# Kernel optimization log

Measured on AMD Instinct MI355X. Metric: run time of the kernel, lower is better.

The kernel has to match this reference:

```python
import jax, jax.numpy as jnp
import numpy as np

COORD_DIM = 4
HIDDEN = 256
N_HIDDEN_LAYERS = 4  # num_layers - 1 hidden->hidden layers after the first
MIN_OMEGA = 10.0
MAX_OMEGA = 100.0
MEDIAN_OMEGA = (MIN_OMEGA + MAX_OMEGA) / 2.0
N = 524288


def _uniform(key, shape, bound):
    return jax.random.uniform(key, shape, jnp.float32, -bound, bound)


def setup_inputs() -> dict:
    key = jax.random.key(0)
    ks = jax.random.split(key, 16)
    coords = jax.random.normal(ks[0], (N, COORD_DIM), jnp.float32)
    # omega predictor: Linear(4, 64) -> ReLU -> Linear(64, 1) -> Sigmoid
    ow1 = _uniform(ks[1], (COORD_DIM, HIDDEN // 4), 1.0 / np.sqrt(COORD_DIM))
    ob1 = _uniform(ks[2], (HIDDEN // 4,), 1.0 / np.sqrt(COORD_DIM))
    ow2 = _uniform(ks[3], (HIDDEN // 4, 1), 1.0 / np.sqrt(HIDDEN // 4))
    ob2 = _uniform(ks[4], (1,), 1.0 / np.sqrt(HIDDEN // 4))
    # SIREN first layer: uniform(-1/in_features, 1/in_features)
    w0 = _uniform(ks[5], (COORD_DIM, HIDDEN), 1.0 / COORD_DIM)
    b0 = _uniform(ks[6], (HIDDEN,), 1.0 / np.sqrt(COORD_DIM))
    # SIREN hidden layers: uniform(-sqrt(6/in)/omega0, ...), stacked [4, 256, 256]
    hb = np.sqrt(6.0 / HIDDEN) / MEDIAN_OMEGA
    wh = _uniform(ks[7], (N_HIDDEN_LAYERS, HIDDEN, HIDDEN), hb)
    bh = _uniform(ks[8], (N_HIDDEN_LAYERS, HIDDEN), 1.0 / np.sqrt(HIDDEN))
    wf = _uniform(ks[9], (HIDDEN, 1), hb)
    bf = _uniform(ks[10], (1,), 1.0 / np.sqrt(HIDDEN))
    return {"coords": coords, "ow1": ow1, "ob1": ob1, "ow2": ow2, "ob2": ob2,
            "w0": w0, "b0": b0, "wh": wh, "bh": bh, "wf": wf, "bf": bf}


def reference(coords, ow1, ob1, ow2, ob2, w0, b0, wh, bh, wf, bf):
    # adaptive omega per coordinate: [N, 1]
    h = jax.nn.relu(coords @ ow1 + ob1)
    omega = MIN_OMEGA + (MAX_OMEGA - MIN_OMEGA) * jax.nn.sigmoid(h @ ow2 + ob2)
    # SIREN stack: x = sin(omega * (x @ W + b))
    x = jnp.sin(omega * (coords @ w0 + b0))
    for i in range(N_HIDDEN_LAYERS):
        x = jnp.sin(omega * (x @ wh[i] + bh[i]))
    return x @ wf + bf  # [N, 1]
```

## Files before the change

### kernel.cpp

```cpp
#include <hip/hip_runtime.h>
#include <hip/hip_bf16.h>

typedef _Float16 f16;
typedef f16 f16x4 __attribute__((ext_vector_type(4)));
typedef f16 f16x8 __attribute__((ext_vector_type(8)));
typedef __fp16 h16x2 __attribute__((ext_vector_type(2)));
typedef __fp16 h16x4 __attribute__((ext_vector_type(4)));
typedef float f32x4 __attribute__((ext_vector_type(4)));
typedef float f32x16 __attribute__((ext_vector_type(16)));

#define MT 64
#define LDST 260
#define INV2PI 0.15915494309189535f

__global__ __launch_bounds__(64)
void prep_wt(const float* __restrict__ wh, f16* __restrict__ wt) {
    const int b = blockIdx.x;
    const int layer = b >> 7, wcblk = (b >> 4) & 7, kblk = b & 15;
    const int lane = threadIdx.x;
    const int l31 = lane & 31, lh = lane >> 5;
    const float* src = wh + layer * 65536 + (kblk * 16 + lh * 8) * 256 + wcblk * 32 + l31;
    f16x8 v;
#pragma unroll
    for (int j = 0; j < 8; j++) v[j] = (f16)src[j * 256];
    *(f16x8*)(wt + b * 512 + lane * 8) = v;
}

__device__ inline f16x8 lds_ld8(const f16* p) {
    f16x4 lo = *(const f16x4*)p;
    f16x4 hi = *(const f16x4*)(p + 4);
    return __builtin_shufflevector(lo, hi, 0, 1, 2, 3, 4, 5, 6, 7);
}

__device__ inline f16x4 pk4(float z0, float z1, float z2, float z3) {
    h16x2 a = __builtin_amdgcn_cvt_pkrtz(z0, z1);
    h16x2 b = __builtin_amdgcn_cvt_pkrtz(z2, z3);
    h16x4 r = __builtin_shufflevector(a, b, 0, 1, 2, 3);
    return __builtin_bit_cast(f16x4, r);
}

__global__ __launch_bounds__(512, 4)
void siren_fused(const float* __restrict__ coords,
                 const float* __restrict__ ow1, const float* __restrict__ ob1,
                 const float* __restrict__ ow2, const float* __restrict__ ob2,
                 const float* __restrict__ w0, const float* __restrict__ b0,
                 const f16* __restrict__ wt,
                 const float* __restrict__ bh,
                 const float* __restrict__ wf,
                 const float* __restrict__ bf,
                 float* __restrict__ out) {
    __shared__ __align__(16) f16 Xs[MT * LDST];
    __shared__ float om_rev[MT];
    __shared__ __align__(16) float crd[MT * 4];
    __shared__ __align__(16) float wf_s[256];

    const int t = threadIdx.x;
    const long base_pt = (long)blockIdx.x * MT;

    const int lane = t & 63;
    const int wave = t >> 6;
    const int l31 = lane & 31;
    const int lh = lane >> 5;
    const int wc0 = wave * 32;

    if (t < MT) ((f32x4*)crd)[t] = ((const f32x4*)(coords + base_pt * 4))[t];
    if (t < 256) wf_s[t] = wf[t];
    __syncthreads();

    {
        const int pt = t >> 3, q = t & 7;
        const float c0 = crd[pt * 4], c1 = crd[pt * 4 + 1], c2 = crd[pt * 4 + 2], c3 = crd[pt * 4 + 3];
        float z2p = 0.f;
#pragma unroll
        for (int jj = 0; jj < 8; jj++) {
            const int j = q * 8 + jj;
            float z = ob1[j] + c0 * ow1[j] + c1 * ow1[64 + j] + c2 * ow1[128 + j] + c3 * ow1[192 + j];
            z2p += fmaxf(z, 0.f) * ow2[j];
        }
        z2p += __shfl_xor(z2p, 1, 64);
        z2p += __shfl_xor(z2p, 2, 64);
        z2p += __shfl_xor(z2p, 4, 64);
        if (q == 0) {
            const float sig = 1.f / (1.f + __expf(-(z2p + ob2[0])));
            om_rev[pt] = (10.f + 90.f * sig) * INV2PI;
        }
    }

    f16x8 a[16];
    {
        const f16* af = wt + ((0 * 8 + wave) * 16) * 512 + lane * 8;
#pragma unroll
        for (int kb = 0; kb < 16; kb++) a[kb] = *(const f16x8*)(af + kb * 512);
    }
    __syncthreads();

    {
        const int pt = t >> 3, q = t & 7;
        const float c0 = crd[pt * 4], c1 = crd[pt * 4 + 1], c2 = crd[pt * 4 + 2], c3 = crd[pt * 4 + 3];
        const float orv = om_rev[pt];
#pragma unroll
        for (int i = 0; i < 2; i++) {
            const int ch0 = (q + 8 * i) * 16;
#pragma unroll
            for (int c = 0; c < 16; c += 4) {
                const int ch = ch0 + c;
                f32x4 wv0 = *(const f32x4*)(w0 + 0 * 256 + ch);
                f32x4 wv1 = *(const f32x4*)(w0 + 1 * 256 + ch);
                f32x4 wv2 = *(const f32x4*)(w0 + 2 * 256 + ch);
                f32x4 wv3 = *(const f32x4*)(w0 + 3 * 256 + ch);
                f32x4 bv  = *(const f32x4*)(b0 + ch);
                float z[4];
#pragma unroll
                for (int j = 0; j < 4; j++) {
                    float zz = bv[j] + c0 * wv0[j] + c1 * wv1[j] + c2 * wv2[j] + c3 * wv3[j];
                    z[j] = __builtin_amdgcn_sinf(orv * zz);
                }
                *(f16x4*)&Xs[pt * LDST + ch] = pk4(z[0], z[1], z[2], z[3]);
            }
        }
    }
    __syncthreads();

#pragma unroll 1
    for (int layer = 0; layer < 4; layer++) {
        f32x16 acc[2];
#pragma unroll
        for (int g = 0; g < 4; g++) {
            f32x4 bb = *(const f32x4*)(bh + layer * 256 + wc0 + g * 8 + lh * 4);
#pragma unroll
            for (int j = 0; j < 4; j++) {
                acc[0][g * 4 + j] = bb[j];
                acc[1][g * 4 + j] = bb[j];
            }
        }

        const f16* bptr = &Xs[l31 * LDST + lh * 8];

#pragma unroll
        for (int kb = 0; kb < 16; kb++) {
            f16x8 bv0 = lds_ld8(bptr + 0 * 32 * LDST + kb * 16);
            f16x8 bv1 = lds_ld8(bptr + 1 * 32 * LDST + kb * 16);
            acc[0] = __builtin_amdgcn_mfma_f32_32x32x16_f16(a[kb], bv0, acc[0], 0, 0, 0);
            acc[1] = __builtin_amdgcn_mfma_f32_32x32x16_f16(a[kb], bv1, acc[1], 0, 0, 0);
        }

        if (layer < 3) {
            const f16* af = wt + (((layer + 1) * 8 + wave) * 16) * 512 + lane * 8;
#pragma unroll
            for (int kb = 0; kb < 16; kb++) a[kb] = *(const f16x8*)(af + kb * 512);
        }
        __syncthreads();

        const float orv0 = om_rev[l31];
        const float orv1 = om_rev[32 + l31];
#pragma unroll
        for (int g = 0; g < 4; g++) {
            const int wc = wc0 + g * 8 + lh * 4;
            float z[4];
#pragma unroll
            for (int j = 0; j < 4; j++) z[j] = __builtin_amdgcn_sinf(orv0 * acc[0][g * 4 + j]);
            *(f16x4*)&Xs[(0 * 32 + l31) * LDST + wc] = pk4(z[0], z[1], z[2], z[3]);
#pragma unroll
            for (int j = 0; j < 4; j++) z[j] = __builtin_amdgcn_sinf(orv1 * acc[1][g * 4 + j]);
            *(f16x4*)&Xs[(1 * 32 + l31) * LDST + wc] = pk4(z[0], z[1], z[2], z[3]);
        }
        __syncthreads();
    }

    {
        const int pt = t >> 3, q = t & 7;
        const f16* xrow = &Xs[pt * LDST];
        float s = 0.f;
#pragma unroll
        for (int i = 0; i < 2; i++) {
            const int ch0 = (q + 8 * i) * 16;
#pragma unroll
            for (int c = 0; c < 16; c += 4) {
                f16x4 xv = *(const f16x4*)(xrow + ch0 + c);
                f32x4 wv = *(const f32x4*)&wf_s[ch0 + c];
                s += (float)xv[0] * wv[0] + (float)xv[1] * wv[1]
                   + (float)xv[2] * wv[2] + (float)xv[3] * wv[3];
            }
        }
        s += __shfl_xor(s, 1, 64);
        s += __shfl_xor(s, 2, 64);
        s += __shfl_xor(s, 4, 64);
        if (q == 0) out[base_pt + pt] = s + bf[0];
    }
}

extern "C" void kernel_launch(void* const* d_in, const int* in_sizes, int n_in,
                              void* d_out, int out_size, void* d_ws, size_t ws_size,
                              hipStream_t stream) {
    (void)in_sizes; (void)n_in; (void)out_size; (void)ws_size;
    const float* coords = (const float*)d_in[0];
    const float* ow1 = (const float*)d_in[1];
    const float* ob1 = (const float*)d_in[2];
    const float* ow2 = (const float*)d_in[3];
    const float* ob2 = (const float*)d_in[4];
    const float* w0  = (const float*)d_in[5];
    const float* b0  = (const float*)d_in[6];
    const float* wh  = (const float*)d_in[7];
    const float* bh  = (const float*)d_in[8];
    const float* wf  = (const float*)d_in[9];
    const float* bf  = (const float*)d_in[10];
    float* out = (float*)d_out;
    f16* wt = (f16*)d_ws;

    prep_wt<<<512, 64, 0, stream>>>(wh, wt);
    siren_fused<<<524288 / MT, 512, 0, stream>>>(coords, ow1, ob1, ow2, ob2,
                                                 w0, b0, wt, bh, wf, bf, out);
}
```

Measured before the change: 473.3 us.

## Halve point tile and stream weight fragments through a 3-deep register ring

After: 560.1 us. 1.18x slower.

```diff
diff --git a/kernel.cpp b/kernel.cpp
--- a/kernel.cpp
+++ b/kernel.cpp
@@ -9,7 +9,7 @@
 typedef float f32x4 __attribute__((ext_vector_type(4)));
 typedef float f32x16 __attribute__((ext_vector_type(16)));
 
-#define MT 64
+#define MT 32
 #define LDST 260
 #define INV2PI 0.15915494309189535f
 
@@ -39,7 +39,7 @@
     return __builtin_bit_cast(f16x4, r);
 }
 
-__global__ __launch_bounds__(512, 4)
+__global__ __launch_bounds__(512, 8)
 void siren_fused(const float* __restrict__ coords,
                  const float* __restrict__ ow1, const float* __restrict__ ob1,
                  const float* __restrict__ ow2, const float* __restrict__ ob2,
@@ -68,123 +68,106 @@
     __syncthreads();
 
     {
-        const int pt = t >> 3, q = t & 7;
+        const int pt = t >> 4, q = t & 15;
         const float c0 = crd[pt * 4], c1 = crd[pt * 4 + 1], c2 = crd[pt * 4 + 2], c3 = crd[pt * 4 + 3];
         float z2p = 0.f;
 #pragma unroll
-        for (int jj = 0; jj < 8; jj++) {
-            const int j = q * 8 + jj;
+        for (int jj = 0; jj < 4; jj++) {
+            const int j = q * 4 + jj;
             float z = ob1[j] + c0 * ow1[j] + c1 * ow1[64 + j] + c2 * ow1[128 + j] + c3 * ow1[192 + j];
             z2p += fmaxf(z, 0.f) * ow2[j];
         }
         z2p += __shfl_xor(z2p, 1, 64);
         z2p += __shfl_xor(z2p, 2, 64);
         z2p += __shfl_xor(z2p, 4, 64);
+        z2p += __shfl_xor(z2p, 8, 64);
         if (q == 0) {
             const float sig = 1.f / (1.f + __expf(-(z2p + ob2[0])));
             om_rev[pt] = (10.f + 90.f * sig) * INV2PI;
         }
     }
-
-    f16x8 a[16];
-    {
-        const f16* af = wt + ((0 * 8 + wave) * 16) * 512 + lane * 8;
-#pragma unroll
-        for (int kb = 0; kb < 16; kb++) a[kb] = *(const f16x8*)(af + kb * 512);
-    }
     __syncthreads();
 
     {
-        const int pt = t >> 3, q = t & 7;
+        const int pt = t >> 4, q = t & 15;
         const float c0 = crd[pt * 4], c1 = crd[pt * 4 + 1], c2 = crd[pt * 4 + 2], c3 = crd[pt * 4 + 3];
         const float orv = om_rev[pt];
 #pragma unroll
-        for (int i = 0; i < 2; i++) {
-            const int ch0 = (q + 8 * i) * 16;
+        for (int c = 0; c < 16; c += 4) {
+            const int ch = q * 16 + c;
+            f32x4 wv0 = *(const f32x4*)(w0 + 0 * 256 + ch);
+            f32x4 wv1 = *(const f32x4*)(w0 + 1 * 256 + ch);
+            f32x4 wv2 = *(const f32x4*)(w0 + 2 * 256 + ch);
+            f32x4 wv3 = *(const f32x4*)(w0 + 3 * 256 + ch);
+            f32x4 bv  = *(const f32x4*)(b0 + ch);
+            float z[4];
 #pragma unroll
-            for (int c = 0; c < 16; c += 4) {
-                const int ch = ch0 + c;
-                f32x4 wv0 = *(const f32x4*)(w0 + 0 * 256 + ch);
-                f32x4 wv1 = *(const f32x4*)(w0 + 1 * 256 + ch);
-                f32x4 wv2 = *(const f32x4*)(w0 + 2 * 256 + ch);
-                f32x4 wv3 = *(const f32x4*)(w0 + 3 * 256 + ch);
-                f32x4 bv  = *(const f32x4*)(b0 + ch);
-                float z[4];
-#pragma unroll
-                for (int j = 0; j < 4; j++) {
-                    float zz = bv[j] + c0 * wv0[j] + c1 * wv1[j] + c2 * wv2[j] + c3 * wv3[j];
-                    z[j] = __builtin_amdgcn_sinf(orv * zz);
-                }
-                *(f16x4*)&Xs[pt * LDST + ch] = pk4(z[0], z[1], z[2], z[3]);
+            for (int j = 0; j < 4; j++) {
+                float zz = bv[j] + c0 * wv0[j] + c1 * wv1[j] + c2 * wv2[j] + c3 * wv3[j];
+                z[j] = __builtin_amdgcn_sinf(orv * zz);
             }
+            *(f16x4*)&Xs[pt * LDST + ch] = pk4(z[0], z[1], z[2], z[3]);
         }
     }
     __syncthreads();
 
 #pragma unroll 1
     for (int layer = 0; layer < 4; layer++) {
-        f32x16 acc[2];
+        f32x16 acc;
 #pragma unroll
         for (int g = 0; g < 4; g++) {
             f32x4 bb = *(const f32x4*)(bh + layer * 256 + wc0 + g * 8 + lh * 4);
 #pragma unroll
-            for (int j = 0; j < 4; j++) {
-                acc[0][g * 4 + j] = bb[j];
-                acc[1][g * 4 + j] = bb[j];
-            }
+            for (int j = 0; j < 4; j++) acc[g * 4 + j] = bb[j];
         }
 
+        const f16* afrag = wt + ((layer * 8 + wave) * 16) * 512 + lane * 8;
         const f16* bptr = &Xs[l31 * LDST + lh * 8];
 
+        f16x8 a[3];
+#pragma unroll
+        for (int d = 0; d < 3; d++) a[d] = *(const f16x8*)(afrag + d * 512);
+
+        __builtin_amdgcn_s_setprio(1);
 #pragma unroll
         for (int kb = 0; kb < 16; kb++) {
-            f16x8 bv0 = lds_ld8(bptr + 0 * 32 * LDST + kb * 16);
-            f16x8 bv1 = lds_ld8(bptr + 1 * 32 * LDST + kb * 16);
-            acc[0] = __builtin_amdgcn_mfma_f32_32x32x16_f16(a[kb], bv0, acc[0], 0, 0, 0);
-            acc[1] = __builtin_amdgcn_mfma_f32_32x32x16_f16(a[kb], bv1, acc[1], 0, 0, 0);
+            const int s = kb % 3;
+            f16x8 av = a[s];
+            if (kb + 3 < 16)
+                a[s] = *(const f16x8*)(afrag + (kb + 3) * 512);
+            f16x8 bv = lds_ld8(bptr + kb * 16);
+            acc = __builtin_amdgcn_mfma_f32_32x32x16_f16(av, bv, acc, 0, 0, 0);
         }
-
-        if (layer < 3) {
-            const f16* af = wt + (((layer + 1) * 8 + wave) * 16) * 512 + lane * 8;
-#pragma unroll
-            for (int kb = 0; kb < 16; kb++) a[kb] = *(const f16x8*)(af + kb * 512);
-        }
+        __builtin_amdgcn_s_setprio(0);
         __syncthreads();
 
-        const float orv0 = om_rev[l31];
-        const float orv1 = om_rev[32 + l31];
+        const float orv = om_rev[l31];
 #pragma unroll
         for (int g = 0; g < 4; g++) {
             const int wc = wc0 + g * 8 + lh * 4;
             float z[4];
 #pragma unroll
-            for (int j = 0; j < 4; j++) z[j] = __builtin_amdgcn_sinf(orv0 * acc[0][g * 4 + j]);
-            *(f16x4*)&Xs[(0 * 32 + l31) * LDST + wc] = pk4(z[0], z[1], z[2], z[3]);
-#pragma unroll
-            for (int j = 0; j < 4; j++) z[j] = __builtin_amdgcn_sinf(orv1 * acc[1][g * 4 + j]);
-            *(f16x4*)&Xs[(1 * 32 + l31) * LDST + wc] = pk4(z[0], z[1], z[2], z[3]);
+            for (int j = 0; j < 4; j++) z[j] = __builtin_amdgcn_sinf(orv * acc[g * 4 + j]);
+            *(f16x4*)&Xs[l31 * LDST + wc] = pk4(z[0], z[1], z[2], z[3]);
         }
         __syncthreads();
     }
 
     {
-        const int pt = t >> 3, q = t & 7;
-        const f16* xrow = &Xs[pt * LDST];
+        const int pt = t >> 4, q = t & 15;
+        const f16* xrow = &Xs[pt * LDST + q * 16];
         float s = 0.f;
 #pragma unroll
-        for (int i = 0; i < 2; i++) {
-            const int ch0 = (q + 8 * i) * 16;
-#pragma unroll
-            for (int c = 0; c < 16; c += 4) {
-                f16x4 xv = *(const f16x4*)(xrow + ch0 + c);
-                f32x4 wv = *(const f32x4*)&wf_s[ch0 + c];
-                s += (float)xv[0] * wv[0] + (float)xv[1] * wv[1]
-                   + (float)xv[2] * wv[2] + (float)xv[3] * wv[3];
-            }
+        for (int c = 0; c < 16; c += 4) {
+            f16x4 xv = *(const f16x4*)(xrow + c);
+            f32x4 wv = *(const f32x4*)&wf_s[q * 16 + c];
+            s += (float)xv[0] * wv[0] + (float)xv[1] * wv[1]
+               + (float)xv[2] * wv[2] + (float)xv[3] * wv[3];
         }
         s += __shfl_xor(s, 1, 64);
         s += __shfl_xor(s, 2, 64);
         s += __shfl_xor(s, 4, 64);
+        s += __shfl_xor(s, 8, 64);
         if (q == 0) out[base_pt + pt] = s + bf[0];
     }
 }
```
